# Kernel tuning notes

Measured on AMD Instinct MI355X. Metric: run time of the kernel, lower is better.

## Reference

```python
import jax, jax.numpy as jnp
import numpy as np

N = 100_000          # nodes
E = 1_600_000        # edges (avg degree 16)
N_GRAPHS = 64        # batched graphs for sum_nodes readout
SLOPE_ATTN = 0.2     # leaky_relu slope on attention logits (GAT standard)
SLOPE_INTER = 0.01   # F.leaky_relu default between layers


def _gat_layer(xn, xe, src, dst, Wn, bn, Wv, bv, We, be, a_s, a_e, a_d, a_b, num_nodes):
    # Multi-head GAT with edge features. Wn:[H,Din,Dz] attn proj, Wv:[H,Din,Do] value proj,
    # We:[H,Ein,De] edge proj. Attention logit = a_s.z_src + a_e.ze + a_d.z_dst + b
    # (equivalent to attn_fc(cat(z_src, ze, z_dst)) without materializing the concat).
    z = jnp.einsum('nd,hdk->nhk', xn, Wn) + bn            # [N,H,Dz]
    v = jnp.einsum('nd,hdk->nhk', xn, Wv) + bv            # [N,H,Do]
    ze = jnp.einsum('ed,hdk->ehk', xe, We) + be           # [E,H,De]
    s = (jnp.einsum('ehk,hk->eh', z[src], a_s)
         + jnp.einsum('ehk,hk->eh', ze, a_e)
         + jnp.einsum('ehk,hk->eh', z[dst], a_d) + a_b)   # [E,H]
    s = jax.nn.leaky_relu(s, SLOPE_ATTN)
    # edge-softmax grouped by destination node (stable)
    m = jax.ops.segment_max(s, dst, num_segments=num_nodes)
    m = jnp.where(jnp.isfinite(m), m, 0.0)
    ex = jnp.exp(s - m[dst])
    den = jax.ops.segment_sum(ex, dst, num_segments=num_nodes)
    alpha = ex / (den[dst] + 1e-9)                        # [E,H]
    h = jax.ops.segment_sum(alpha[..., None] * v[src], dst, num_segments=num_nodes)  # [N,H,Do]
    Eh, H, De = ze.shape
    return h.reshape(num_nodes, -1), ze.reshape(Eh, H * De)


def setup_inputs() -> dict:
    key = jax.random.key(0)
    ks = jax.random.split(key, 32)
    f = lambda i, shape: jax.random.normal(ks[i], shape, dtype=jnp.float32) * 0.1
    return dict(
        node_types=f(0, (N, 14)),
        node_labels=f(1, (N, 50)),
        edge_labels=f(2, (E, 32)),
        src=jax.random.randint(ks[3], (E,), 0, N),
        dst=jax.random.randint(ks[4], (E,), 0, N),
        graph_ids=jnp.sort(jax.random.randint(ks[5], (N,), 0, N_GRAPHS)),
        l0_Wn=f(6, (2, 64, 32)), l0_bn=f(7, (2, 32)),
        l0_Wv=f(8, (2, 64, 64)), l0_bv=f(9, (2, 64)),
        l0_We=f(10, (2, 32, 16)), l0_be=f(11, (2, 16)),
        l0_as=f(12, (2, 32)), l0_ae=f(13, (2, 16)), l0_ad=f(14, (2, 32)), l0_ab=f(15, (2,)),
        l1_Wn=f(16, (2, 128, 32)), l1_bn=f(17, (2, 32)),
        l1_Wv=f(18, (2, 128, 64)), l1_bv=f(19, (2, 64)),
        l1_We=f(20, (2, 32, 16)), l1_be=f(21, (2, 16)),
        l1_as=f(22, (2, 32)), l1_ae=f(23, (2, 16)), l1_ad=f(24, (2, 32)), l1_ab=f(25, (2,)),
        fc_W=f(26, (128, 2)), fc_b=f(27, (2,)),
    )


def reference(node_types, node_labels, edge_labels, src, dst, graph_ids,
              l0_Wn, l0_bn, l0_Wv, l0_bv, l0_We, l0_be, l0_as, l0_ae, l0_ad, l0_ab,
              l1_Wn, l1_bn, l1_Wv, l1_bv, l1_We, l1_be, l1_as, l1_ae, l1_ad, l1_ab,
              fc_W, fc_b):
    xn = jnp.concatenate([node_types, node_labels], axis=1)   # node_features_use == 'all'
    xe = edge_labels
    xn, xe = _gat_layer(xn, xe, src, dst, l0_Wn, l0_bn, l0_Wv, l0_bv,
                        l0_We, l0_be, l0_as, l0_ae, l0_ad, l0_ab, N)
    xn = jax.nn.leaky_relu(xn, SLOPE_INTER)
    xe = jax.nn.leaky_relu(xe, SLOPE_INTER)
    xn, xe = _gat_layer(xn, xe, src, dst, l1_Wn, l1_bn, l1_Wv, l1_bv,
                        l1_We, l1_be, l1_as, l1_ae, l1_ad, l1_ab, N)
    # dgl.sum_nodes over batched graphs, then classification FC
    graph_sum = jax.ops.segment_sum(xn, graph_ids, num_segments=N_GRAPHS)  # [G, 128]
    return graph_sum @ fc_W + fc_b
```

## Files before the change

kernel.cpp:

```cpp
#include <hip/hip_runtime.h>

#define NN 100000
#define EE 1600000
#define NG 64

#define BSH 9
#define NWIN 512
#define NB 196
#define CAP 10240
#define EPB 4096

#define OFF_WS0 0
#define OFF_WD0 128
#define OFF_CS0 256
#define OFF_CD0 258
#define OFF_U1  260
#define OFF_C1  324
#define OFF_WS1 512
#define OFF_WD1 768
#define OFF_CS1 1024
#define OFF_CD1 1026
#define OFF_WT0 2048
#define FOLD_FLOATS 4096

typedef __attribute__((ext_vector_type(8))) short short8;
typedef __attribute__((ext_vector_type(4))) float f32x4;

__device__ __forceinline__ unsigned encm(float f) {
  unsigned u = __float_as_uint(f);
  return (u & 0x80000000u) ? ~u : (u | 0x80000000u);
}
__device__ __forceinline__ float decm(unsigned u) {
  return (u & 0x80000000u) ? __uint_as_float(u & 0x7FFFFFFFu) : __uint_as_float(~u);
}
__device__ __forceinline__ unsigned bf16r(float f) {
  unsigned u = __float_as_uint(f);
  return (u + 0x7FFFu + ((u >> 16) & 1u)) >> 16;
}

__global__ void fold_k(const float* __restrict__ Wn0, const float* __restrict__ bn0,
                       const float* __restrict__ as0, const float* __restrict__ ad0,
                       const float* __restrict__ We0,
                       const float* __restrict__ We1, const float* __restrict__ be1,
                       const float* __restrict__ ae1,
                       const float* __restrict__ Wn1, const float* __restrict__ bn1,
                       const float* __restrict__ as1, const float* __restrict__ ad1,
                       const float* __restrict__ Wv1,
                       float* __restrict__ fold, unsigned* __restrict__ w1tw) {
  int t = threadIdx.x;
  for (int i = t; i < 128; i += 256) {
    int h = i >> 6, d = i & 63;
    float s = 0.f, sd = 0.f;
    for (int k = 0; k < 32; ++k) {
      float w = Wn0[h*2048 + d*32 + k];
      s  += w * as0[h*32 + k];
      sd += w * ad0[h*32 + k];
    }
    fold[OFF_WS0 + i] = s; fold[OFF_WD0 + i] = sd;
  }
  for (int i = t; i < 64; i += 256) {
    int h = i >> 5, d = i & 31;
    float s = 0.f;
    for (int k = 0; k < 16; ++k) s += We1[h*512 + d*16 + k] * ae1[h*16 + k];
    fold[OFF_U1 + i] = s;
  }
  for (int i = t; i < 1024; i += 256) {
    int o = i >> 5, d = i & 31;
    fold[OFF_WT0 + o*32 + d] = We0[(o >> 4)*512 + d*16 + (o & 15)];
  }
  for (int i = t; i < 8192; i += 256) {
    int o = i >> 6, dw = i & 63;
    int d0 = 2*dw, d1 = d0 + 1;
    float f0 = Wv1[(o >> 6)*8192 + d0*64 + (o & 63)];
    float f1 = Wv1[(o >> 6)*8192 + d1*64 + (o & 63)];
    w1tw[i] = bf16r(f0) | (bf16r(f1) << 16);
  }
  if (t < 256) {
    int i = t, h = i >> 7, d = i & 127;
    float s = 0.f, sd = 0.f;
    for (int k = 0; k < 32; ++k) {
      float w = Wn1[h*4096 + d*32 + k];
      s  += w * as1[h*32 + k];
      sd += w * ad1[h*32 + k];
    }
    fold[OFF_WS1 + i] = s; fold[OFF_WD1 + i] = sd;
  }
  if (t < 2) {
    float cs = 0.f, cd = 0.f;
    for (int k = 0; k < 32; ++k) { cs += bn0[t*32+k]*as0[t*32+k]; cd += bn0[t*32+k]*ad0[t*32+k]; }
    fold[OFF_CS0 + t] = cs; fold[OFF_CD0 + t] = cd;
    float c1 = 0.f;
    for (int k = 0; k < 16; ++k) c1 += ae1[t*16+k]*be1[t*16+k];
    fold[OFF_C1 + t] = c1;
    float cs1 = 0.f, cd1 = 0.f;
    for (int k = 0; k < 32; ++k) { cs1 += bn1[t*32+k]*as1[t*32+k]; cd1 += bn1[t*32+k]*ad1[t*32+k]; }
    fold[OFF_CS1 + t] = cs1; fold[OFF_CD1 + t] = cd1;
  }
}

__global__ __launch_bounds__(256) void binA_k(const int* __restrict__ dst,
                                              int* __restrict__ bcur, uint2* __restrict__ stg) {
  __shared__ int hist[NB], gbase[NB];
  int tid = threadIdx.x;
  for (int i = tid; i < NB; i += 256) hist[i] = 0;
  __syncthreads();
  int e0 = blockIdx.x*EPB;
  int dd[16], li[16];
  #pragma unroll
  for (int q = 0; q < 16; ++q) {
    int e = e0 + q*256 + tid;
    if (e < EE) {
      int dn = dst[e];
      dd[q] = dn;
      li[q] = atomicAdd(&hist[dn >> BSH], 1);
    }
  }
  __syncthreads();
  if (tid < NB) gbase[tid] = atomicAdd(&bcur[tid], hist[tid]);
  __syncthreads();
  #pragma unroll
  for (int q = 0; q < 16; ++q) {
    int e = e0 + q*256 + tid;
    if (e < EE) {
      int b = dd[q] >> BSH;
      int idx = gbase[b] + li[q];
      if (idx < CAP) stg[(size_t)b*CAP + idx] = make_uint2((unsigned)e, (unsigned)dd[q]);
    }
  }
}

__global__ void scanB_k(const int* __restrict__ bcur, int* __restrict__ bbase) {
  int s = 0;
  for (int b = 0; b < NB; ++b) { bbase[b] = s; s += bcur[b]; }
}

__global__ __launch_bounds__(256) void binB_k(const uint2* __restrict__ stg, const int* __restrict__ bcur,
                                              const int* __restrict__ bbase,
                                              int* __restrict__ off, int* __restrict__ eid,
                                              int* __restrict__ dnp) {
  __shared__ int hist[NWIN], curx[NWIN], wsum[4];
  int tid = threadIdx.x, lane = tid & 63, w = tid >> 6;
  int b = blockIdx.x;
  int nbase = b << BSH;
  int cnt = bcur[b], base = bbase[b];
  for (int i = tid; i < NWIN; i += 256) hist[i] = 0;
  __syncthreads();
  const uint2* sp = stg + (size_t)b*CAP;
  for (int i = tid; i < cnt; i += 256) atomicAdd(&hist[sp[i].y - nbase], 1);
  __syncthreads();
  int a0 = hist[2*tid], a1 = hist[2*tid + 1];
  int tsum = a0 + a1;
  int x = tsum;
  #pragma unroll
  for (int o = 1; o < 64; o <<= 1) { int y = __shfl_up(x, o); if (lane >= o) x += y; }
  if (lane == 63) wsum[w] = x;
  __syncthreads();
  if (tid == 0) { int s = 0; for (int q = 0; q < 4; ++q) { int t = wsum[q]; wsum[q] = s; s += t; } }
  __syncthreads();
  int excl = wsum[w] + x - tsum;
  curx[2*tid]     = base + excl;
  curx[2*tid + 1] = base + excl + a0;
  __syncthreads();
  for (int j = tid; j < NWIN; j += 256) {
    int n = nbase + j;
    if (n < NN) off[n] = curx[j];
  }
  if (b == NB - 1 && tid == 0) off[NN] = base + cnt;
  __syncthreads();
  for (int i = tid; i < cnt; i += 256) {
    uint2 r = sp[i];
    int p = atomicAdd(&curx[r.y - nbase], 1);
    eid[p] = (int)r.x;
    dnp[p] = (int)r.y;
  }
}

__global__ __launch_bounds__(128) void node0v_k(const float* __restrict__ nt, const float* __restrict__ nl,
                                                const float* __restrict__ Wv0, const float* __restrict__ bv0,
                                                unsigned* __restrict__ v0b) {
  int tid = threadIdx.x;
  int h = tid >> 6, k = tid & 63;
  int sl2 = k & 31;
  float w[64];
  #pragma unroll
  for (int d = 0; d < 64; ++d) w[d] = Wv0[h*4096 + d*64 + k];
  float b = bv0[tid];
  int nb = blockIdx.x * 8;
  #pragma unroll 1
  for (int r = 0; r < 8; ++r) {
    int n = nb + r;
    const float* nrow = nt + (size_t)n*14;
    const float* lrow = nl + (size_t)n*50;
    float acc = b;
    #pragma unroll
    for (int d = 0; d < 14; ++d) acc = fmaf(nrow[d], w[d], acc);
    #pragma unroll
    for (int d = 0; d < 50; ++d) acc = fmaf(lrow[d], w[14 + d], acc);
    float p0 = __shfl(acc, 2*sl2);
    float p1 = __shfl(acc, 2*sl2 + 1);
    if (k < 32) v0b[(size_t)n*64 + h*32 + sl2] = bf16r(p0) | (bf16r(p1) << 16);
  }
}

__global__ __launch_bounds__(256) void nodez_k(const float* __restrict__ nt, const float* __restrict__ nl,
                                               const float* __restrict__ fold,
                                               float* __restrict__ zs0, float* __restrict__ zd0) {
  int n = blockIdx.x*256 + threadIdx.x;
  if (n >= NN) return;
  float p0 = 0.f, p1 = 0.f, p2 = 0.f, p3 = 0.f;
  #pragma unroll
  for (int d = 0; d < 64; ++d) {
    float x = (d < 14) ? nt[(size_t)n*14 + d] : nl[(size_t)n*50 + d - 14];
    p0 = fmaf(x, fold[OFF_WS0 + d],      p0);
    p1 = fmaf(x, fold[OFF_WS0 + 64 + d], p1);
    p2 = fmaf(x, fold[OFF_WD0 + d],      p2);
    p3 = fmaf(x, fold[OFF_WD0 + 64 + d], p3);
  }
  zs0[n*2]   = p0 + fold[OFF_CS0];
  zs0[n*2+1] = p1 + fold[OFF_CS0+1];
  zd0[n*2]   = p2 + fold[OFF_CD0];
  zd0[n*2+1] = p3 + fold[OFF_CD0+1];
}

__global__ __launch_bounds__(256) void edge0_k(const float* __restrict__ xe,
                                               const int* __restrict__ src,
                                               const int* __restrict__ eid, const int* __restrict__ dnp,
                                               const float* __restrict__ be0,
                                               const float* __restrict__ ae0, const float* __restrict__ ab0,
                                               const float* __restrict__ fold,
                                               const float* __restrict__ zs0, const float* __restrict__ zd0,
                                               float4* __restrict__ ebuf, float* __restrict__ et1p,
                                               unsigned* __restrict__ menc0) {
  int p = blockIdx.x*256 + threadIdx.x;
  int lane = threadIdx.x & 63;
  int e = eid[p];
  int dn = dnp[p];
  int sn = src[e];
  const float4* xp = reinterpret_cast<const float4*>(xe + (size_t)e*32);
  float4 xv[8];
  #pragma unroll
  for (int q = 0; q < 8; ++q) xv[q] = xp[q];
  const float* WT = fold + OFF_WT0;
  const float* U1 = fold + OFF_U1;
  float s0 = 0.f, s1 = 0.f, etA = 0.f, etB = 0.f;
  #pragma unroll 4
  for (int o = 0; o < 16; ++o) {
    float acc = be0[o];
    #pragma unroll
    for (int q = 0; q < 8; ++q) {
      float4 w = *reinterpret_cast<const float4*>(WT + o*32 + q*4);
      acc = fmaf(xv[q].x, w.x, acc); acc = fmaf(xv[q].y, w.y, acc);
      acc = fmaf(xv[q].z, w.z, acc); acc = fmaf(xv[q].w, w.w, acc);
    }
    s0 = fmaf(ae0[o], acc, s0);
    float lz = acc >= 0.f ? acc : 0.01f*acc;
    etA = fmaf(lz, U1[o], etA); etB = fmaf(lz, U1[32 + o], etB);
  }
  #pragma unroll 4
  for (int o = 16; o < 32; ++o) {
    float acc = be0[o];
    #pragma unroll
    for (int q = 0; q < 8; ++q) {
      float4 w = *reinterpret_cast<const float4*>(WT + o*32 + q*4);
      acc = fmaf(xv[q].x, w.x, acc); acc = fmaf(xv[q].y, w.y, acc);
      acc = fmaf(xv[q].z, w.z, acc); acc = fmaf(xv[q].w, w.w, acc);
    }
    s1 = fmaf(ae0[o], acc, s1);
    float lz = acc >= 0.f ? acc : 0.01f*acc;
    etA = fmaf(lz, U1[o], etA); etB = fmaf(lz, U1[32 + o], etB);
  }
  float2 zsv = *reinterpret_cast<const float2*>(zs0 + (size_t)sn*2);
  float2 zdv = *reinterpret_cast<const float2*>(zd0 + (size_t)dn*2);
  float l0 = zsv.x + s0 + zdv.x + ab0[0];
  float l1 = zsv.y + s1 + zdv.y + ab0[1];
  l0 = l0 >= 0.f ? l0 : 0.2f*l0;
  l1 = l1 >= 0.f ? l1 : 0.2f*l1;
  ebuf[p] = make_float4(__int_as_float(sn), l0, l1, __int_as_float(dn));
  *reinterpret_cast<float2*>(et1p + (size_t)p*2) =
      make_float2(etA + fold[OFF_C1], etB + fold[OFF_C1+1]);
  unsigned e0 = encm(l0), e1 = encm(l1);
  #pragma unroll
  for (int o = 1; o < 64; o <<= 1) {
    int pdn = __shfl_down(dn, o);
    unsigned q0 = __shfl_down(e0, o);
    unsigned q1 = __shfl_down(e1, o);
    if (pdn == dn) { e0 = max(e0, q0); e1 = max(e1, q1); }
  }
  int prev = __shfl_up(dn, 1);
  if (lane == 0 || prev != dn) {
    atomicMax(&menc0[(size_t)dn*2],   e0);
    atomicMax(&menc0[(size_t)dn*2+1], e1);
  }
}

__global__ __launch_bounds__(256) void agg0_k(const int* __restrict__ off,
                                              const float4* __restrict__ ebuf,
                                              const unsigned* __restrict__ menc,
                                              const unsigned* __restrict__ v0b,
                                              const float* __restrict__ fold,
                                              unsigned* __restrict__ xb,
                                              float* __restrict__ zs1, float* __restrict__ zd1) {
  int tid = threadIdx.x, w = tid >> 6, lane = tid & 63;
  int n = blockIdx.x*4 + w;
  int head = lane >> 5;
  int st = off[n], en = off[n+1];
  float m = decm(menc[(size_t)n*2 + head]);
  float alo = 0.f, ahi = 0.f, den = 0.f;
  for (int i = st; i < en; i += 8) {
    float4 eb[8]; unsigned vr[8];
    #pragma unroll
    for (int q = 0; q < 8; ++q) { int j = i + q; eb[q] = ebuf[(j < en) ? j : st]; }
    #pragma unroll
    for (int q = 0; q < 8; ++q) vr[q] = v0b[(size_t)__float_as_int(eb[q].x)*64 + lane];
    #pragma unroll
    for (int q = 0; q < 8; ++q) {
      bool ok = (i + q) < en;
      float s = head ? eb[q].z : eb[q].y;
      float e = ok ? __expf(s - m) : 0.f;
      den += e;
      alo = fmaf(e, __uint_as_float(vr[q] << 16),         alo);
      ahi = fmaf(e, __uint_as_float(vr[q] & 0xFFFF0000u), ahi);
    }
  }
  float inv = 1.f / (den + 1e-9f);
  float xlo = alo*inv, xhi = ahi*inv;
  xlo = xlo >= 0.f ? xlo : 0.01f*xlo;
  xhi = xhi >= 0.f ? xhi : 0.01f*xhi;
  xb[(size_t)n*64 + lane] = bf16r(xlo) | (bf16r(xhi) << 16);
  const float2* ws1 = reinterpret_cast<const float2*>(fold + OFF_WS1);
  const float2* wd1 = reinterpret_cast<const float2*>(fold + OFF_WD1);
  float2 wa = ws1[lane], wb = ws1[64 + lane], wc = wd1[lane], wd = wd1[64 + lane];
  float p0 = xlo*wa.x + xhi*wa.y;
  float p1 = xlo*wb.x + xhi*wb.y;
  float p2 = xlo*wc.x + xhi*wc.y;
  float p3 = xlo*wd.x + xhi*wd.y;
  #pragma unroll
  for (int o = 32; o > 0; o >>= 1) {
    p0 += __shfl_down(p0, o); p1 += __shfl_down(p1, o);
    p2 += __shfl_down(p2, o); p3 += __shfl_down(p3, o);
  }
  if (lane == 0) {
    zs1[n*2]   = p0 + fold[OFF_CS1];
    zs1[n*2+1] = p1 + fold[OFF_CS1+1];
    zd1[n*2]   = p2 + fold[OFF_CD1];
    zd1[n*2+1] = p3 + fold[OFF_CD1+1];
  }
}

__global__ __launch_bounds__(256) void node1m_k(const unsigned* __restrict__ xb,
                                                const unsigned* __restrict__ w1tw,
                                                const float* __restrict__ bv1,
                                                unsigned short* __restrict__ v1s) {
  int tid = threadIdx.x, w = tid >> 6, lane = tid & 63;
  int tile = blockIdx.x*4 + w;
  if (tile >= NN/16) return;
  int row = lane & 15, kg = lane >> 4;
  int n = tile*16 + row;
  short8 a[4];
  #pragma unroll
  for (int ks = 0; ks < 4; ++ks)
    a[ks] = *reinterpret_cast<const short8*>(xb + (size_t)n*64 + ks*16 + kg*4);
  #pragma unroll 2
  for (int t = 0; t < 8; ++t) {
    float bias = bv1[t*16 + row];
    f32x4 acc = {bias, bias, bias, bias};
    #pragma unroll
    for (int ks = 0; ks < 4; ++ks) {
      short8 b = *reinterpret_cast<const short8*>(w1tw + (size_t)(t*16 + row)*64 + ks*16 + kg*4);
      acc = __builtin_amdgcn_mfma_f32_16x16x32_bf16(a[ks], b, acc, 0, 0, 0);
    }
    int o = t*16 + row;
    #pragma unroll
    for (int r = 0; r < 4; ++r) {
      int nr = tile*16 + kg*4 + r;
      v1s[(size_t)nr*128 + o] = (unsigned short)bf16r(acc[r]);
    }
  }
}

__global__ __launch_bounds__(256) void edge1_k(float4* __restrict__ ebuf,
                                               const float* __restrict__ zs1, const float* __restrict__ zd1,
                                               const float* __restrict__ et1p, const float* __restrict__ ab1,
                                               unsigned* __restrict__ menc1) {
  int i = blockIdx.x*256 + threadIdx.x;
  int lane = threadIdx.x & 63;
  bool ok = i < EE;
  float l0 = 0.f, l1 = 0.f; int dn = -1;
  if (ok) {
    float4 eb = ebuf[i];
    int sn = __float_as_int(eb.x);
    dn = __float_as_int(eb.w);
    float2 et = *reinterpret_cast<const float2*>(et1p + (size_t)i*2);
    l0 = zs1[sn*2]   + et.x + zd1[dn*2]   + ab1[0];
    l1 = zs1[sn*2+1] + et.y + zd1[dn*2+1] + ab1[1];
    l0 = l0 >= 0.f ? l0 : 0.2f*l0;
    l1 = l1 >= 0.f ? l1 : 0.2f*l1;
    eb.y = l0; eb.z = l1;
    ebuf[i] = eb;
  }
  unsigned e0 = ok ? encm(l0) : 0u;
  unsigned e1 = ok ? encm(l1) : 0u;
  #pragma unroll
  for (int o = 1; o < 64; o <<= 1) {
    int pdn = __shfl_down(dn, o);
    unsigned q0 = __shfl_down(e0, o);
    unsigned q1 = __shfl_down(e1, o);
    if (pdn == dn) { e0 = max(e0, q0); e1 = max(e1, q1); }
  }
  int prev = __shfl_up(dn, 1);
  if (ok && (lane == 0 || prev != dn)) {
    atomicMax(&menc1[(size_t)dn*2],   e0);
    atomicMax(&menc1[(size_t)dn*2+1], e1);
  }
}

__global__ void outinit_k(const float* __restrict__ fcb, float* __restrict__ out) {
  int i = threadIdx.x;
  out[i] = fcb[i & 1];
}

__global__ __launch_bounds__(256) void agg1_k(const int* __restrict__ off,
                                              const float4* __restrict__ ebuf,
                                              const unsigned* __restrict__ menc,
                                              const unsigned* __restrict__ v1b,
                                              const float* __restrict__ fcW,
                                              float* __restrict__ pnode) {
  int tid = threadIdx.x, w = tid >> 6, lane = tid & 63;
  int n = blockIdx.x*4 + w;
  int head = lane >> 5;
  int st = off[n], en = off[n+1];
  float m = decm(menc[(size_t)n*2 + head]);
  float alo = 0.f, ahi = 0.f, den = 0.f;
  for (int i = st; i < en; i += 8) {
    float4 eb[8]; unsigned vr[8];
    #pragma unroll
    for (int q = 0; q < 8; ++q) { int j = i + q; eb[q] = ebuf[(j < en) ? j : st]; }
    #pragma unroll
    for (int q = 0; q < 8; ++q) vr[q] = v1b[(size_t)__float_as_int(eb[q].x)*64 + lane];
    #pragma unroll
    for (int q = 0; q < 8; ++q) {
      bool ok = (i + q) < en;
      float s = head ? eb[q].z : eb[q].y;
      float e = ok ? __expf(s - m) : 0.f;
      den += e;
      alo = fmaf(e, __uint_as_float(vr[q] << 16),         alo);
      ahi = fmaf(e, __uint_as_float(vr[q] & 0xFFFF0000u), ahi);
    }
  }
  float inv = 1.f / (den + 1e-9f);
  float hlo = alo*inv, hhi = ahi*inv;
  const float2* fw2 = reinterpret_cast<const float2*>(fcW);
  float2 f0 = fw2[2*lane], f1 = fw2[2*lane + 1];
  float p0 = hlo*f0.x + hhi*f1.x;
  float p1 = hlo*f0.y + hhi*f1.y;
  #pragma unroll
  for (int o = 32; o > 0; o >>= 1) {
    p0 += __shfl_down(p0, o);
    p1 += __shfl_down(p1, o);
  }
  if (lane == 0) {
    pnode[n*2]   = p0;
    pnode[n*2+1] = p1;
  }
}

__global__ __launch_bounds__(256) void gsum_k(const float* __restrict__ pnode, const int* __restrict__ gid,
                                              float* __restrict__ out) {
  int n = blockIdx.x*256 + threadIdx.x;
  int lane = threadIdx.x & 63;
  bool ok = n < NN;
  int g = ok ? gid[n] : -1;
  float p0 = ok ? pnode[n*2]   : 0.f;
  float p1 = ok ? pnode[n*2+1] : 0.f;
  #pragma unroll
  for (int o = 1; o < 64; o <<= 1) {
    int pg = __shfl_down(g, o);
    float q0 = __shfl_down(p0, o);
    float q1 = __shfl_down(p1, o);
    if ((lane + o) < 64 && pg == g) { p0 += q0; p1 += q1; }
  }
  int prev = __shfl_up(g, 1);
  if (ok && (lane == 0 || prev != g)) {
    atomicAdd(&out[g*2],     p0);
    atomicAdd(&out[g*2 + 1], p1);
  }
}

extern "C" void kernel_launch(void* const* d_in, const int* in_sizes, int n_in,
                              void* d_out, int out_size, void* d_ws, size_t ws_size,
                              hipStream_t stream) {
  const float* nt  = (const float*)d_in[0];
  const float* nl  = (const float*)d_in[1];
  const float* xe  = (const float*)d_in[2];
  const int*   src = (const int*)d_in[3];
  const int*   dst = (const int*)d_in[4];
  const int*   gid = (const int*)d_in[5];
  const float* Wn0 = (const float*)d_in[6],  *bn0 = (const float*)d_in[7];
  const float* Wv0 = (const float*)d_in[8],  *bv0 = (const float*)d_in[9];
  const float* We0 = (const float*)d_in[10], *be0 = (const float*)d_in[11];
  const float* as0 = (const float*)d_in[12], *ae0 = (const float*)d_in[13];
  const float* ad0 = (const float*)d_in[14], *ab0 = (const float*)d_in[15];
  const float* Wn1 = (const float*)d_in[16], *bn1 = (const float*)d_in[17];
  const float* Wv1 = (const float*)d_in[18], *bv1 = (const float*)d_in[19];
  const float* We1 = (const float*)d_in[20], *be1 = (const float*)d_in[21];
  const float* as1 = (const float*)d_in[22], *ae1 = (const float*)d_in[23];
  const float* ad1 = (const float*)d_in[24], *ab1 = (const float*)d_in[25];
  const float* fcW = (const float*)d_in[26], *fcb = (const float*)d_in[27];
  float* out = (float*)d_out;

  float* fold  = (float*)d_ws;
  float* zs    = fold + FOLD_FLOATS;
  float* zd    = zs + (size_t)NN*2;
  unsigned* v0b = (unsigned*)(zd + (size_t)NN*2);
  unsigned* v1b = v0b + (size_t)NN*64;
  unsigned* xb  = v1b + (size_t)NN*64;
  unsigned* w1tw = xb + (size_t)NN*64;
  float* et1p  = (float*)(w1tw + 128*64);
  float* ebuff = et1p + (size_t)EE*2;
  unsigned* menc0 = (unsigned*)(ebuff + (size_t)EE*4);
  unsigned* menc1 = menc0 + (size_t)NN*2;
  int* bcur   = (int*)(menc1 + (size_t)NN*2);
  int* bbase  = bcur + NB;
  float* pnode = (float*)(bbase + NB);
  int* off    = (int*)(pnode + (size_t)NN*2);
  int* eid    = off + NN + 1;
  int* dnp    = eid + EE;
  uint2* stg  = (uint2*)(dnp + EE);
  float4* ebuf = (float4*)ebuff;

  hipMemsetAsync(menc0, 0, ((size_t)NN*4 + NB)*sizeof(unsigned), stream);
  fold_k<<<1, 256, 0, stream>>>(Wn0, bn0, as0, ad0, We0, We1, be1, ae1, Wn1, bn1, as1, ad1, Wv1, fold, w1tw);
  binA_k<<<(EE + EPB - 1)/EPB, 256, 0, stream>>>(dst, bcur, stg);
  scanB_k<<<1, 1, 0, stream>>>(bcur, bbase);
  binB_k<<<NB, 256, 0, stream>>>(stg, bcur, bbase, off, eid, dnp);
  node0v_k<<<NN/8, 128, 0, stream>>>(nt, nl, Wv0, bv0, v0b);
  nodez_k<<<(NN + 255)/256, 256, 0, stream>>>(nt, nl, fold, zs, zd);
  edge0_k<<<EE/256, 256, 0, stream>>>(xe, src, eid, dnp, be0, ae0, ab0, fold, zs, zd, ebuf, et1p, menc0);
  agg0_k<<<NN/4, 256, 0, stream>>>(off, ebuf, menc0, v0b, fold, xb, zs, zd);
  node1m_k<<<(NN/16 + 3)/4, 256, 0, stream>>>(xb, w1tw, bv1, (unsigned short*)v1b);
  edge1_k<<<EE/256, 256, 0, stream>>>(ebuf, zs, zd, et1p, ab1, menc1);
  outinit_k<<<1, 128, 0, stream>>>(fcb, out);
  agg1_k<<<NN/4, 256, 0, stream>>>(off, ebuf, menc1, v1b, fcW, pnode);
  gsum_k<<<(NN + 255)/256, 256, 0, stream>>>(pnode, gid, out);
}
```

Measured before the change: 479.1 us.

## Fuse layer-1 edge logit and max into aggregation kernel, drop edge1 pass

Removes the separate edge1 kernel. The layer-1 attention logits and the per-destination max are now computed inside agg1 from zs1, zd1, et1p and the source indices in the CSR-ordered edge buffer. The max uses the monotonicity of leaky_relu: it takes the raw max first and applies the constant destination term afterwards. This removes a full edge pass, the atomics and the menc1 buffer and its memset, at the cost of each aggregation warp reading edge data twice. The tail handling in agg0 and agg1 also switches from clamped redundant loads to predicated loads.

```diff
diff --git a/kernel.cpp b/kernel.cpp
--- a/kernel.cpp
+++ b/kernel.cpp
@@ -275,7 +275,7 @@
   float l1 = zsv.y + s1 + zdv.y + ab0[1];
   l0 = l0 >= 0.f ? l0 : 0.2f*l0;
   l1 = l1 >= 0.f ? l1 : 0.2f*l1;
-  ebuf[p] = make_float4(__int_as_float(sn), l0, l1, __int_as_float(dn));
+  ebuf[p] = make_float4(__int_as_float(sn), l0, l1, 0.f);
   *reinterpret_cast<float2*>(et1p + (size_t)p*2) =
       make_float2(etA + fold[OFF_C1], etB + fold[OFF_C1+1]);
   unsigned e0 = encm(l0), e1 = encm(l1);
@@ -307,19 +307,21 @@
   float m = decm(menc[(size_t)n*2 + head]);
   float alo = 0.f, ahi = 0.f, den = 0.f;
   for (int i = st; i < en; i += 8) {
+    int nv = en - i;
     float4 eb[8]; unsigned vr[8];
     #pragma unroll
-    for (int q = 0; q < 8; ++q) { int j = i + q; eb[q] = ebuf[(j < en) ? j : st]; }
-    #pragma unroll
-    for (int q = 0; q < 8; ++q) vr[q] = v0b[(size_t)__float_as_int(eb[q].x)*64 + lane];
+    for (int q = 0; q < 8; ++q) if (q < nv) eb[q] = ebuf[i + q];
+    #pragma unroll
+    for (int q = 0; q < 8; ++q) if (q < nv) vr[q] = v0b[(size_t)__float_as_int(eb[q].x)*64 + lane];
     #pragma unroll
     for (int q = 0; q < 8; ++q) {
-      bool ok = (i + q) < en;
-      float s = head ? eb[q].z : eb[q].y;
-      float e = ok ? __expf(s - m) : 0.f;
-      den += e;
-      alo = fmaf(e, __uint_as_float(vr[q] << 16),         alo);
-      ahi = fmaf(e, __uint_as_float(vr[q] & 0xFFFF0000u), ahi);
+      if (q < nv) {
+        float s = head ? eb[q].z : eb[q].y;
+        float e = __expf(s - m);
+        den += e;
+        alo = fmaf(e, __uint_as_float(vr[q] << 16),         alo);
+        ahi = fmaf(e, __uint_as_float(vr[q] & 0xFFFF0000u), ahi);
+      }
     }
   }
   float inv = 1.f / (den + 1e-9f);
@@ -378,42 +380,6 @@
   }
 }
 
-__global__ __launch_bounds__(256) void edge1_k(float4* __restrict__ ebuf,
-                                               const float* __restrict__ zs1, const float* __restrict__ zd1,
-                                               const float* __restrict__ et1p, const float* __restrict__ ab1,
-                                               unsigned* __restrict__ menc1) {
-  int i = blockIdx.x*256 + threadIdx.x;
-  int lane = threadIdx.x & 63;
-  bool ok = i < EE;
-  float l0 = 0.f, l1 = 0.f; int dn = -1;
-  if (ok) {
-    float4 eb = ebuf[i];
-    int sn = __float_as_int(eb.x);
-    dn = __float_as_int(eb.w);
-    float2 et = *reinterpret_cast<const float2*>(et1p + (size_t)i*2);
-    l0 = zs1[sn*2]   + et.x + zd1[dn*2]   + ab1[0];
-    l1 = zs1[sn*2+1] + et.y + zd1[dn*2+1] + ab1[1];
-    l0 = l0 >= 0.f ? l0 : 0.2f*l0;
-    l1 = l1 >= 0.f ? l1 : 0.2f*l1;
-    eb.y = l0; eb.z = l1;
-    ebuf[i] = eb;
-  }
-  unsigned e0 = ok ? encm(l0) : 0u;
-  unsigned e1 = ok ? encm(l1) : 0u;
-  #pragma unroll
-  for (int o = 1; o < 64; o <<= 1) {
-    int pdn = __shfl_down(dn, o);
-    unsigned q0 = __shfl_down(e0, o);
-    unsigned q1 = __shfl_down(e1, o);
-    if (pdn == dn) { e0 = max(e0, q0); e1 = max(e1, q1); }
-  }
-  int prev = __shfl_up(dn, 1);
-  if (ok && (lane == 0 || prev != dn)) {
-    atomicMax(&menc1[(size_t)dn*2],   e0);
-    atomicMax(&menc1[(size_t)dn*2+1], e1);
-  }
-}
-
 __global__ void outinit_k(const float* __restrict__ fcb, float* __restrict__ out) {
   int i = threadIdx.x;
   out[i] = fcb[i & 1];
@@ -421,7 +387,9 @@
 
 __global__ __launch_bounds__(256) void agg1_k(const int* __restrict__ off,
                                               const float4* __restrict__ ebuf,
-                                              const unsigned* __restrict__ menc,
+                                              const float* __restrict__ et1p,
+                                              const float* __restrict__ zs1, const float* __restrict__ zd1,
+                                              const float* __restrict__ ab1,
                                               const unsigned* __restrict__ v1b,
                                               const float* __restrict__ fcW,
                                               float* __restrict__ pnode) {
@@ -429,22 +397,43 @@
   int n = blockIdx.x*4 + w;
   int head = lane >> 5;
   int st = off[n], en = off[n+1];
-  float m = decm(menc[(size_t)n*2 + head]);
+  float cnode = zd1[(size_t)n*2 + head] + ab1[head];
+  float mraw = -1e30f;
+  for (int i = st; i < en; i += 8) {
+    int nv = en - i;
+    #pragma unroll
+    for (int q = 0; q < 8; ++q) {
+      if (q < nv) {
+        int sn = __float_as_int(ebuf[i + q].x);
+        float s = zs1[(size_t)sn*2 + head] + et1p[(size_t)(i + q)*2 + head];
+        mraw = fmaxf(mraw, s);
+      }
+    }
+  }
+  float m = mraw + cnode;
+  m = m >= 0.f ? m : 0.2f*m;
   float alo = 0.f, ahi = 0.f, den = 0.f;
   for (int i = st; i < en; i += 8) {
-    float4 eb[8]; unsigned vr[8];
-    #pragma unroll
-    for (int q = 0; q < 8; ++q) { int j = i + q; eb[q] = ebuf[(j < en) ? j : st]; }
-    #pragma unroll
-    for (int q = 0; q < 8; ++q) vr[q] = v1b[(size_t)__float_as_int(eb[q].x)*64 + lane];
+    int nv = en - i;
+    float sr[8]; unsigned vr[8];
     #pragma unroll
     for (int q = 0; q < 8; ++q) {
-      bool ok = (i + q) < en;
-      float s = head ? eb[q].z : eb[q].y;
-      float e = ok ? __expf(s - m) : 0.f;
-      den += e;
-      alo = fmaf(e, __uint_as_float(vr[q] << 16),         alo);
-      ahi = fmaf(e, __uint_as_float(vr[q] & 0xFFFF0000u), ahi);
+      if (q < nv) {
+        int sn = __float_as_int(ebuf[i + q].x);
+        vr[q] = v1b[(size_t)sn*64 + lane];
+        sr[q] = zs1[(size_t)sn*2 + head] + et1p[(size_t)(i + q)*2 + head];
+      }
+    }
+    #pragma unroll
+    for (int q = 0; q < 8; ++q) {
+      if (q < nv) {
+        float l = sr[q] + cnode;
+        l = l >= 0.f ? l : 0.2f*l;
+        float e = __expf(l - m);
+        den += e;
+        alo = fmaf(e, __uint_as_float(vr[q] << 16),         alo);
+        ahi = fmaf(e, __uint_as_float(vr[q] & 0xFFFF0000u), ahi);
+      }
     }
   }
   float inv = 1.f / (den + 1e-9f);
@@ -518,8 +507,7 @@
   float* et1p  = (float*)(w1tw + 128*64);
   float* ebuff = et1p + (size_t)EE*2;
   unsigned* menc0 = (unsigned*)(ebuff + (size_t)EE*4);
-  unsigned* menc1 = menc0 + (size_t)NN*2;
-  int* bcur   = (int*)(menc1 + (size_t)NN*2);
+  int* bcur   = (int*)(menc0 + (size_t)NN*2);
   int* bbase  = bcur + NB;
   float* pnode = (float*)(bbase + NB);
   int* off    = (int*)(pnode + (size_t)NN*2);
@@ -528,7 +516,7 @@
   uint2* stg  = (uint2*)(dnp + EE);
   float4* ebuf = (float4*)ebuff;
 
-  hipMemsetAsync(menc0, 0, ((size_t)NN*4 + NB)*sizeof(unsigned), stream);
+  hipMemsetAsync(menc0, 0, ((size_t)NN*2 + NB)*sizeof(unsigned), stream);
   fold_k<<<1, 256, 0, stream>>>(Wn0, bn0, as0, ad0, We0, We1, be1, ae1, Wn1, bn1, as1, ad1, Wv1, fold, w1tw);
   binA_k<<<(EE + EPB - 1)/EPB, 256, 0, stream>>>(dst, bcur, stg);
   scanB_k<<<1, 1, 0, stream>>>(bcur, bbase);
@@ -538,8 +526,7 @@
   edge0_k<<<EE/256, 256, 0, stream>>>(xe, src, eid, dnp, be0, ae0, ab0, fold, zs, zd, ebuf, et1p, menc0);
   agg0_k<<<NN/4, 256, 0, stream>>>(off, ebuf, menc0, v0b, fold, xb, zs, zd);
   node1m_k<<<(NN/16 + 3)/4, 256, 0, stream>>>(xb, w1tw, bv1, (unsigned short*)v1b);
-  edge1_k<<<EE/256, 256, 0, stream>>>(ebuf, zs, zd, et1p, ab1, menc1);
   outinit_k<<<1, 128, 0, stream>>>(fcb, out);
-  agg1_k<<<NN/4, 256, 0, stream>>>(off, ebuf, menc1, v1b, fcW, pnode);
+  agg1_k<<<NN/4, 256, 0, stream>>>(off, ebuf, et1p, zs, zd, ab1, v1b, fcW, pnode);
   gsum_k<<<(NN + 255)/256, 256, 0, stream>>>(pnode, gid, out);
 }
```

Result: slower. 701.4 us (+46.4%).
